# Performance work log

Hardware: AMD Instinct MI355X
Metric: run time of the kernel (lower is better)

The kernel has to match this reference:

```python
import jax, jax.numpy as jnp
import numpy as np

B, S, N, D = 4, 1024, 16, 512
H, HD = 8, 64
THETA = 10000.0


def setup_inputs() -> dict:
    key = jax.random.key(0)
    k0, k1, k2, k3 = jax.random.split(key, 4)
    x = jax.random.normal(k0, (B, S, N, D), dtype=jnp.float32)
    pos_bias = jax.random.normal(k1, (H, N, N), dtype=jnp.float32)
    W_qkv = jax.random.normal(k2, (D, 3 * H * HD), dtype=jnp.float32) / np.sqrt(D).astype(np.float32)
    W_out = jax.random.normal(k3, (H * HD, D), dtype=jnp.float32) / np.sqrt(H * HD).astype(np.float32)
    # mixed mask (not all True -> no early-return path; not all False -> masking active)
    focus_present_mask = jnp.array([True, False, True, False])
    return {"x": x, "pos_bias": pos_bias, "W_qkv": W_qkv, "W_out": W_out,
            "focus_present_mask": focus_present_mask}


def _rotary_cos_sin(n, d, dtype):
    # rotary-embedding-torch: inv_freq over even indices, each freq repeated twice adjacently
    inv_freq = 1.0 / (THETA ** (jnp.arange(0, d, 2, dtype=jnp.float32) / d))
    freqs = jnp.arange(n, dtype=jnp.float32)[:, None] * inv_freq  # (n, d/2)
    freqs = jnp.repeat(freqs, 2, axis=-1)                          # (n, d)
    return jnp.cos(freqs).astype(dtype), jnp.sin(freqs).astype(dtype)


def _rotate_half(t):
    # pairs (x0, x1) -> (-x1, x0), interleaved layout
    t2 = t.reshape(*t.shape[:-1], t.shape[-1] // 2, 2)
    t2 = jnp.stack([-t2[..., 1], t2[..., 0]], axis=-1)
    return t2.reshape(t.shape)


def reference(x, pos_bias, W_qkv, W_out, focus_present_mask):
    scale = HD ** -0.5
    n = x.shape[-2]
    qkv = x @ W_qkv                                   # (b, s, n, 3*h*hd)
    q, k, v = jnp.split(qkv, 3, axis=-1)

    def to_heads(t):  # (..., n, h*hd) -> (..., h, n, hd)
        return t.reshape(*t.shape[:-1], H, HD).swapaxes(-2, -3)

    q = to_heads(q) * scale
    k = to_heads(k)
    v = to_heads(v)

    cos, sin = _rotary_cos_sin(n, HD, q.dtype)
    q = q * cos + _rotate_half(q) * sin
    k = k * cos + _rotate_half(k) * sin

    sim = jnp.einsum('bshid,bshjd->bshij', q, k)      # (b, s, h, n, n)
    sim = sim + pos_bias                              # broadcast (h, n, n)

    eye = jnp.eye(n, dtype=bool)
    ones = jnp.ones((n, n), dtype=bool)
    mask = jnp.where(focus_present_mask[:, None, None, None, None],
                     eye[None, None, None], ones[None, None, None])
    sim = jnp.where(mask, sim, -jnp.finfo(sim.dtype).max)

    attn = jax.nn.softmax(sim, axis=-1)
    out = jnp.einsum('bshij,bshjd->bshid', attn, v)   # (b, s, h, n, hd)
    out = out.swapaxes(-2, -3).reshape(*x.shape[:-1], H * HD)
    return out @ W_out
```

## Files before the change

### kernel.cpp

```cpp
#include <hip/hip_runtime.h>
#include <cstdint>

#define BB   4
#define SS   1024
#define NTOK 16
#define DD   512
#define HH   8
#define HD   64
#define M_TOTAL (BB * SS * NTOK)
#define QKV_COLS (3 * HH * HD)

typedef unsigned short u16;
typedef short bf16x8 __attribute__((ext_vector_type(8)));
typedef float f32x4 __attribute__((ext_vector_type(4)));

__device__ __forceinline__ float bf2f(u16 u) {
  union { uint32_t i; float f; } x; x.i = ((uint32_t)u) << 16; return x.f;
}
__device__ __forceinline__ u16 f2bf(float f) {
  union { uint32_t i; float f; } x; x.f = f;
  uint32_t i = x.i;
  if ((i & 0x7fffffffu) > 0x7f800000u) return 0x7fc0;
  uint32_t r = (i + 0x7fffu + ((i >> 16) & 1u)) >> 16;
  return (u16)r;
}

__device__ __forceinline__ bool decode_mask(const void* p, int b) {
  uint32_t w0 = *(const uint32_t*)p;
  if (w0 == 0x00010001u) return ((const uint8_t*)p)[b] != 0;
  if (w0 == 0x00003F80u) return ((const u16*)p)[b] != 0;
  if (w0 == 0x3F800000u) return ((const float*)p)[b] != 0.0f;
  return ((const int32_t*)p)[b] != 0;
}

__global__ void sniff_kernel(const u16* __restrict__ x, int* __restrict__ flag) {
  __shared__ int any;
  if (threadIdx.x == 0) any = 0;
  __syncthreads();
  int cnt = 0;
  for (int i = threadIdx.x; i < 8192; i += 256) {
    int e = (x[i] >> 7) & 0xFF;
    if (e >= 141) cnt++;
  }
  if (cnt) atomicOr(&any, 1);
  __syncthreads();
  if (threadIdx.x == 0) *flag = any ? 1 : 0;
}

__global__ void rot_table_kernel(float* __restrict__ cosv, float* __restrict__ sinv) {
  for (int p = threadIdx.x; p < NTOK * 32; p += 256) {
    int n = p >> 5, i = p & 31;
    float ang = (float)n * powf(10000.0f, -(float)(2 * i) / 64.0f);
    cosv[p] = cosf(ang);
    sinv[p] = sinf(ang);
  }
}

__global__ __launch_bounds__(256) void cast_x_kernel(
    const void* __restrict__ src, u16* __restrict__ dst, size_t elem_off,
    const int* __restrict__ flag) {
  size_t i = ((size_t)blockIdx.x * 256 + threadIdx.x) * 4;
  ushort4 o;
  if (*flag) {
    float4 v = *(const float4*)((const float*)src + elem_off + i);
    o.x = f2bf(v.x); o.y = f2bf(v.y); o.z = f2bf(v.z); o.w = f2bf(v.w);
  } else {
    o = *(const ushort4*)((const u16*)src + elem_off + i);
  }
  *(ushort4*)(dst + i) = o;
}

__global__ __launch_bounds__(256) void cast_wt_kernel(
    const void* __restrict__ W, u16* __restrict__ WT, int K, int N,
    const int* __restrict__ flag) {
  size_t idx = (size_t)blockIdx.x * 256 + threadIdx.x;
  int n = (int)(idx / K), k = (int)(idx % K);
  float v = (*flag) ? ((const float*)W)[(size_t)k * N + n]
                    : bf2f(((const u16*)W)[(size_t)k * N + n]);
  WT[idx] = f2bf(v);
}

template <int OUT_F32>
__global__ __launch_bounds__(256) void gemm_mfma_bt(
    const u16* __restrict__ A, const u16* __restrict__ BT, void* __restrict__ Cbase,
    size_t c_elem_off, int M, int N, int K, const int* __restrict__ flag) {
  __shared__ u16 Asl[128 * 32];
  __shared__ u16 Bsl[128 * 32];
  const int tid  = threadIdx.x;
  const int wave = tid >> 6;
  const int lane = tid & 63;
  const int bm = blockIdx.y * 128;
  const int bn = blockIdx.x * 128;
  const int wm = (wave >> 1) * 64;
  const int wn = (wave & 1) * 64;
  const int m_lane = lane & 15;
  const int kgrp   = lane >> 4;

  f32x4 acc[4][4];
#pragma unroll
  for (int r = 0; r < 4; ++r)
#pragma unroll
    for (int c = 0; c < 4; ++c) acc[r][c] = (f32x4){0.f, 0.f, 0.f, 0.f};

  for (int k0 = 0; k0 < K; k0 += 32) {
#pragma unroll
    for (int q = 0; q < 2; ++q) {
      const int idx = q * 256 + tid;
      const int row = idx >> 2;
      const int gc  = (idx & 3) ^ (row & 3);
      const u16* ga = A  + (size_t)(bm + row) * K + k0 + gc * 8;
      const u16* gb = BT + (size_t)(bn + row) * K + k0 + gc * 8;
      u16* la = Asl + (size_t)(q * 256 + wave * 64) * 8;
      u16* lb = Bsl + (size_t)(q * 256 + wave * 64) * 8;
      __builtin_amdgcn_global_load_lds(
          (const __attribute__((address_space(1))) void*)ga,
          (__attribute__((address_space(3))) void*)la, 16, 0, 0);
      __builtin_amdgcn_global_load_lds(
          (const __attribute__((address_space(1))) void*)gb,
          (__attribute__((address_space(3))) void*)lb, 16, 0, 0);
    }
    __syncthreads();

    bf16x8 af[4], bfr[4];
#pragma unroll
    for (int r = 0; r < 4; ++r) {
      const int ra = wm + r * 16 + m_lane;
      af[r] = *(const bf16x8*)(Asl + ra * 32 + ((kgrp ^ (ra & 3)) * 8));
    }
#pragma unroll
    for (int c = 0; c < 4; ++c) {
      const int rb = wn + c * 16 + m_lane;
      bfr[c] = *(const bf16x8*)(Bsl + rb * 32 + ((kgrp ^ (rb & 3)) * 8));
    }
#pragma unroll
    for (int r = 0; r < 4; ++r)
#pragma unroll
      for (int c = 0; c < 4; ++c)
        acc[r][c] = __builtin_amdgcn_mfma_f32_16x16x32_bf16(af[r], bfr[c], acc[r][c], 0, 0, 0);
    __syncthreads();
  }

  const bool f32out = OUT_F32 && (*flag != 0);
#pragma unroll
  for (int r = 0; r < 4; ++r) {
    const int grow0 = bm + wm + r * 16 + kgrp * 4;
#pragma unroll
    for (int c = 0; c < 4; ++c) {
      const int gcol = bn + wn + c * 16 + m_lane;
#pragma unroll
      for (int j = 0; j < 4; ++j) {
        const size_t off = c_elem_off + (size_t)(grow0 + j) * N + gcol;
        if (f32out) ((float*)Cbase)[off] = acc[r][c][j];
        else        ((u16*)Cbase)[off]   = f2bf(acc[r][c][j]);
      }
    }
  }
}

__global__ __launch_bounds__(256) void attn_kernel(
    const u16* __restrict__ qkv, const void* __restrict__ pos_bias,
    const void* __restrict__ maskp, u16* __restrict__ attno, int bs0,
    const float* __restrict__ cosv, const float* __restrict__ sinv,
    const int* __restrict__ flag) {
  const int bid = blockIdx.x;
  const int h = bid & (HH - 1);
  const int bsl = bid >> 3;
  const int b = (bs0 + bsl) >> 10;

  __shared__ float qs[NTOK][HD];
  __shared__ float ks[NTOK][HD + 1];
  __shared__ float vs[NTOK][HD];
  __shared__ float sim[NTOK][NTOK + 1];

  const int tid = threadIdx.x;
  const int n = tid >> 4;
  const int e = (tid & 15) * 4;

  size_t rowbase = ((size_t)bsl * NTOK + n) * QKV_COLS + h * HD + e;
  ushort4 uq = *(const ushort4*)(qkv + rowbase);
  ushort4 uk = *(const ushort4*)(qkv + rowbase + 512);
  ushort4 uv = *(const ushort4*)(qkv + rowbase + 1024);
  qs[n][e + 0] = bf2f(uq.x); qs[n][e + 1] = bf2f(uq.y);
  qs[n][e + 2] = bf2f(uq.z); qs[n][e + 3] = bf2f(uq.w);
  ks[n][e + 0] = bf2f(uk.x); ks[n][e + 1] = bf2f(uk.y);
  ks[n][e + 2] = bf2f(uk.z); ks[n][e + 3] = bf2f(uk.w);
  vs[n][e + 0] = bf2f(uv.x); vs[n][e + 1] = bf2f(uv.y);
  vs[n][e + 2] = bf2f(uv.z); vs[n][e + 3] = bf2f(uv.w);
  __syncthreads();

  for (int p = tid; p < NTOK * 32; p += 256) {
    int nn = p >> 5, i = p & 31;
    float c = cosv[p], s = sinv[p];
    float q0 = qs[nn][2 * i], q1 = qs[nn][2 * i + 1];
    qs[nn][2 * i]     = (q0 * c - q1 * s) * 0.125f;
    qs[nn][2 * i + 1] = (q1 * c + q0 * s) * 0.125f;
    float k0 = ks[nn][2 * i], k1 = ks[nn][2 * i + 1];
    ks[nn][2 * i]     = k0 * c - k1 * s;
    ks[nn][2 * i + 1] = k1 * c + k0 * s;
  }
  __syncthreads();

  const int i = tid >> 4, j = tid & 15;
  float acc = 0.0f;
#pragma unroll
  for (int d = 0; d < HD; ++d) acc += qs[i][d] * ks[j][d];
  size_t pbidx = ((size_t)h * NTOK + i) * NTOK + j;
  acc += (*flag) ? ((const float*)pos_bias)[pbidx]
                 : bf2f(((const u16*)pos_bias)[pbidx]);
  bool focus = decode_mask(maskp, b);
  if (focus && (i != j)) acc = -3.0e38f;
  sim[i][j] = acc;
  __syncthreads();

  if (tid < NTOK) {
    float m = -3.4e38f;
#pragma unroll
    for (int jj = 0; jj < NTOK; ++jj) m = fmaxf(m, sim[tid][jj]);
    float ssum = 0.0f;
#pragma unroll
    for (int jj = 0; jj < NTOK; ++jj) {
      float ex = expf(sim[tid][jj] - m);
      sim[tid][jj] = ex;
      ssum += ex;
    }
    float inv = 1.0f / ssum;
#pragma unroll
    for (int jj = 0; jj < NTOK; ++jj) sim[tid][jj] *= inv;
  }
  __syncthreads();

  float o0 = 0, o1 = 0, o2 = 0, o3 = 0;
#pragma unroll
  for (int jj = 0; jj < NTOK; ++jj) {
    float p = sim[n][jj];
    o0 += p * vs[jj][e + 0];
    o1 += p * vs[jj][e + 1];
    o2 += p * vs[jj][e + 2];
    o3 += p * vs[jj][e + 3];
  }
  size_t obase = ((size_t)bsl * NTOK + n) * (HH * HD) + h * HD + e;
  ushort4 uo;
  uo.x = f2bf(o0); uo.y = f2bf(o1); uo.z = f2bf(o2); uo.w = f2bf(o3);
  *(ushort4*)(attno + obase) = uo;
}

extern "C" void kernel_launch(void* const* d_in, const int* in_sizes, int n_in,
                              void* d_out, int out_size, void* d_ws, size_t ws_size,
                              hipStream_t stream) {
  const void* x_raw    = d_in[0];
  const void* pos_bias = d_in[1];
  const void* W_qkv    = d_in[2];
  const void* W_out    = d_in[3];
  const void* maskp    = d_in[4];

  char* ws = (char*)d_ws;
  int*   flag = (int*)ws;
  float* cosv = (float*)(ws + 256);
  float* sinv = cosv + NTOK * 32;
  u16* WqT = (u16*)(ws + 256 + 4096);
  u16* WoT = WqT + (size_t)QKV_COLS * DD;
  u16* scratch = WoT + (size_t)DD * DD;
  const size_t fixed = 256 + 4096 + (size_t)QKV_COLS * DD * 2 + (size_t)DD * DD * 2;
  const size_t ws_avail = (ws_size > fixed) ? ws_size - fixed : 0;

  const size_t per_row = 5120;
  int chunk_rows = M_TOTAL;
  while ((size_t)chunk_rows * per_row > ws_avail && chunk_rows > 128) chunk_rows >>= 1;
  const int nchunks = M_TOTAL / chunk_rows;

  u16* xb    = scratch;
  u16* qkv   = xb  + (size_t)chunk_rows * DD;
  u16* attno = qkv + (size_t)chunk_rows * QKV_COLS;

  sniff_kernel<<<1, 256, 0, stream>>>((const u16*)x_raw, flag);
  rot_table_kernel<<<1, 256, 0, stream>>>(cosv, sinv);
  cast_wt_kernel<<<(QKV_COLS * DD) / 256, 256, 0, stream>>>(W_qkv, WqT, DD, QKV_COLS, flag);
  cast_wt_kernel<<<(DD * DD) / 256, 256, 0, stream>>>(W_out, WoT, DD, DD, flag);

  for (int c = 0; c < nchunks; ++c) {
    const int bs0 = c * (chunk_rows / NTOK);
    const size_t eoff = (size_t)c * chunk_rows * DD;

    cast_x_kernel<<<(int)(((size_t)chunk_rows * DD) / 1024), 256, 0, stream>>>(
        x_raw, xb, eoff, flag);

    {
      dim3 grid(QKV_COLS / 128, chunk_rows / 128);
      gemm_mfma_bt<0><<<grid, 256, 0, stream>>>(xb, WqT, (void*)qkv, 0,
                                                chunk_rows, QKV_COLS, DD, flag);
    }
    {
      dim3 grid((chunk_rows / NTOK) * HH);
      attn_kernel<<<grid, 256, 0, stream>>>(qkv, pos_bias, maskp, attno, bs0,
                                            cosv, sinv, flag);
    }
    {
      dim3 grid(DD / 128, chunk_rows / 128);
      gemm_mfma_bt<1><<<grid, 256, 0, stream>>>(attno, WoT, d_out, eoff,
                                                chunk_rows, DD, DD, flag);
    }
  }
}
```

Baseline: 628.0 us.

## Rewrite attention kernel as one wave per (row, head) using bf16 MFMA

The attention kernel now gives each wavefront a single (b,s,head) 16x16 problem, with four per block, instead of one block per problem. QK^T and PV are computed with 16x16x32 bf16 MFMA instructions, and softmax is reduced with cross-lane shuffles rather than through shared memory and block barriers. Rotary cos/sin tables are staged in LDS. This removes most __syncthreads and scalar FMA work, at the cost of rounding rotated q/k and the probabilities to bf16, plus strided uncoalesced V loads.

```diff
diff --git a/kernel.cpp b/kernel.cpp
--- a/kernel.cpp
+++ b/kernel.cpp
@@ -162,86 +162,119 @@
     const void* __restrict__ maskp, u16* __restrict__ attno, int bs0,
     const float* __restrict__ cosv, const float* __restrict__ sinv,
     const int* __restrict__ flag) {
-  const int bid = blockIdx.x;
-  const int h = bid & (HH - 1);
-  const int bsl = bid >> 3;
+  __shared__ float lcos[NTOK * 33];
+  __shared__ float lsin[NTOK * 33];
+  const int tid = threadIdx.x;
+  for (int p = tid; p < NTOK * 32; p += 256) {
+    int n = p >> 5, i = p & 31;
+    lcos[n * 33 + i] = cosv[p];
+    lsin[n * 33 + i] = sinv[p];
+  }
+  __syncthreads();
+
+  const int wave = tid >> 6;
+  const int lane = tid & 63;
+  const int wid = blockIdx.x * 4 + wave;
+  const int bsl = wid >> 3;
+  const int h = wid & (HH - 1);
   const int b = (bs0 + bsl) >> 10;
-
-  __shared__ float qs[NTOK][HD];
-  __shared__ float ks[NTOK][HD + 1];
-  __shared__ float vs[NTOK][HD];
-  __shared__ float sim[NTOK][NTOK + 1];
-
-  const int tid = threadIdx.x;
-  const int n = tid >> 4;
-  const int e = (tid & 15) * 4;
-
-  size_t rowbase = ((size_t)bsl * NTOK + n) * QKV_COLS + h * HD + e;
-  ushort4 uq = *(const ushort4*)(qkv + rowbase);
-  ushort4 uk = *(const ushort4*)(qkv + rowbase + 512);
-  ushort4 uv = *(const ushort4*)(qkv + rowbase + 1024);
-  qs[n][e + 0] = bf2f(uq.x); qs[n][e + 1] = bf2f(uq.y);
-  qs[n][e + 2] = bf2f(uq.z); qs[n][e + 3] = bf2f(uq.w);
-  ks[n][e + 0] = bf2f(uk.x); ks[n][e + 1] = bf2f(uk.y);
-  ks[n][e + 2] = bf2f(uk.z); ks[n][e + 3] = bf2f(uk.w);
-  vs[n][e + 0] = bf2f(uv.x); vs[n][e + 1] = bf2f(uv.y);
-  vs[n][e + 2] = bf2f(uv.z); vs[n][e + 3] = bf2f(uv.w);
-  __syncthreads();
-
-  for (int p = tid; p < NTOK * 32; p += 256) {
-    int nn = p >> 5, i = p & 31;
-    float c = cosv[p], s = sinv[p];
-    float q0 = qs[nn][2 * i], q1 = qs[nn][2 * i + 1];
-    qs[nn][2 * i]     = (q0 * c - q1 * s) * 0.125f;
-    qs[nn][2 * i + 1] = (q1 * c + q0 * s) * 0.125f;
-    float k0 = ks[nn][2 * i], k1 = ks[nn][2 * i + 1];
-    ks[nn][2 * i]     = k0 * c - k1 * s;
-    ks[nn][2 * i + 1] = k1 * c + k0 * s;
-  }
-  __syncthreads();
-
-  const int i = tid >> 4, j = tid & 15;
-  float acc = 0.0f;
-#pragma unroll
-  for (int d = 0; d < HD; ++d) acc += qs[i][d] * ks[j][d];
-  size_t pbidx = ((size_t)h * NTOK + i) * NTOK + j;
-  acc += (*flag) ? ((const float*)pos_bias)[pbidx]
-                 : bf2f(((const u16*)pos_bias)[pbidx]);
-  bool focus = decode_mask(maskp, b);
-  if (focus && (i != j)) acc = -3.0e38f;
-  sim[i][j] = acc;
-  __syncthreads();
-
-  if (tid < NTOK) {
-    float m = -3.4e38f;
-#pragma unroll
-    for (int jj = 0; jj < NTOK; ++jj) m = fmaxf(m, sim[tid][jj]);
-    float ssum = 0.0f;
-#pragma unroll
-    for (int jj = 0; jj < NTOK; ++jj) {
-      float ex = expf(sim[tid][jj] - m);
-      sim[tid][jj] = ex;
-      ssum += ex;
-    }
-    float inv = 1.0f / ssum;
-#pragma unroll
-    for (int jj = 0; jj < NTOK; ++jj) sim[tid][jj] *= inv;
-  }
-  __syncthreads();
-
-  float o0 = 0, o1 = 0, o2 = 0, o3 = 0;
-#pragma unroll
-  for (int jj = 0; jj < NTOK; ++jj) {
-    float p = sim[n][jj];
-    o0 += p * vs[jj][e + 0];
-    o1 += p * vs[jj][e + 1];
-    o2 += p * vs[jj][e + 2];
-    o3 += p * vs[jj][e + 3];
-  }
-  size_t obase = ((size_t)bsl * NTOK + n) * (HH * HD) + h * HD + e;
-  ushort4 uo;
-  uo.x = f2bf(o0); uo.y = f2bf(o1); uo.z = f2bf(o2); uo.w = f2bf(o3);
-  *(ushort4*)(attno + obase) = uo;
+  const int qt = lane & 15;
+  const int kg = lane >> 4;
+
+  const u16* rowp = qkv + ((size_t)bsl * NTOK + qt) * QKV_COLS + h * HD;
+  float qv[16], kv[16];
+#pragma unroll
+  for (int hf = 0; hf < 2; ++hf) {
+    const bf16x8 uq = *(const bf16x8*)(rowp + hf * 32 + kg * 8);
+    const bf16x8 uk = *(const bf16x8*)(rowp + 512 + hf * 32 + kg * 8);
+#pragma unroll
+    for (int t = 0; t < 8; ++t) {
+      qv[hf * 8 + t] = bf2f((u16)uq[t]);
+      kv[hf * 8 + t] = bf2f((u16)uk[t]);
+    }
+  }
+
+  const u16* vbase = qkv + (size_t)bsl * NTOK * QKV_COLS + 1024 + h * HD;
+  u16 vraw[32];
+#pragma unroll
+  for (int mt = 0; mt < 4; ++mt)
+#pragma unroll
+    for (int t = 0; t < 8; ++t)
+      vraw[mt * 8 + t] = (kg < 2)
+          ? vbase[(size_t)(kg * 8 + t) * QKV_COLS + mt * 16 + qt]
+          : (u16)0;
+
+  bf16x8 qa[2], ka[2];
+#pragma unroll
+  for (int hf = 0; hf < 2; ++hf) {
+#pragma unroll
+    for (int t = 0; t < 4; ++t) {
+      const int idx = qt * 33 + hf * 16 + kg * 4 + t;
+      const float cth = lcos[idx], sth = lsin[idx];
+      const int e0 = hf * 8 + 2 * t, e1 = e0 + 1;
+      const float q0 = qv[e0], q1 = qv[e1];
+      qa[hf][2 * t]     = (short)f2bf((q0 * cth - q1 * sth) * 0.125f);
+      qa[hf][2 * t + 1] = (short)f2bf((q1 * cth + q0 * sth) * 0.125f);
+      const float k0 = kv[e0], k1 = kv[e1];
+      ka[hf][2 * t]     = (short)f2bf(k0 * cth - k1 * sth);
+      ka[hf][2 * t + 1] = (short)f2bf(k1 * cth + k0 * sth);
+    }
+  }
+
+  f32x4 cacc = (f32x4){0.f, 0.f, 0.f, 0.f};
+  cacc = __builtin_amdgcn_mfma_f32_16x16x32_bf16(ka[0], qa[0], cacc, 0, 0, 0);
+  cacc = __builtin_amdgcn_mfma_f32_16x16x32_bf16(ka[1], qa[1], cacc, 0, 0, 0);
+
+  const bool f32pb = (*flag != 0);
+  const bool focus = decode_mask(maskp, b);
+  float sv[4];
+#pragma unroll
+  for (int j = 0; j < 4; ++j) {
+    const int kt = kg * 4 + j;
+    const size_t pbidx = ((size_t)h * NTOK + qt) * NTOK + kt;
+    const float pb = f32pb ? ((const float*)pos_bias)[pbidx]
+                           : bf2f(((const u16*)pos_bias)[pbidx]);
+    float v = cacc[j] + pb;
+    if (focus && (qt != kt)) v = -3.0e38f;
+    sv[j] = v;
+  }
+
+  float m = fmaxf(fmaxf(sv[0], sv[1]), fmaxf(sv[2], sv[3]));
+  m = fmaxf(m, __shfl_xor(m, 16, 64));
+  m = fmaxf(m, __shfl_xor(m, 32, 64));
+  float pj[4];
+  float ssum = 0.f;
+#pragma unroll
+  for (int j = 0; j < 4; ++j) {
+    pj[j] = expf(sv[j] - m);
+    ssum += pj[j];
+  }
+  ssum += __shfl_xor(ssum, 16, 64);
+  ssum += __shfl_xor(ssum, 32, 64);
+  const float inv = 1.0f / ssum;
+#pragma unroll
+  for (int j = 0; j < 4; ++j) pj[j] *= inv;
+
+  bf16x8 pfrag;
+#pragma unroll
+  for (int t = 0; t < 8; ++t) {
+    const int src = (lane & 15) + (((kg << 1) + (t >> 2)) << 4);
+    const float v = __shfl(pj[t & 3], src & 63, 64);
+    pfrag[t] = (kg < 2) ? (short)f2bf(v) : (short)0;
+  }
+
+  u16* orow = attno + ((size_t)bsl * NTOK + qt) * (HH * HD) + h * HD;
+#pragma unroll
+  for (int mt = 0; mt < 4; ++mt) {
+    bf16x8 vfrag;
+#pragma unroll
+    for (int t = 0; t < 8; ++t) vfrag[t] = (short)vraw[mt * 8 + t];
+    f32x4 o = (f32x4){0.f, 0.f, 0.f, 0.f};
+    o = __builtin_amdgcn_mfma_f32_16x16x32_bf16(vfrag, pfrag, o, 0, 0, 0);
+    ushort4 uo;
+    uo.x = f2bf(o[0]); uo.y = f2bf(o[1]); uo.z = f2bf(o[2]); uo.w = f2bf(o[3]);
+    *(ushort4*)(orow + mt * 16 + kg * 4) = uo;
+  }
 }
 
 extern "C" void kernel_launch(void* const* d_in, const int* in_sizes, int n_in,
@@ -290,7 +323,7 @@
                                                 chunk_rows, QKV_COLS, DD, flag);
     }
     {
-      dim3 grid((chunk_rows / NTOK) * HH);
+      dim3 grid(((chunk_rows / NTOK) * HH) / 4);
       attn_kernel<<<grid, 256, 0, stream>>>(qkv, pos_bias, maskp, attno, bs0,
                                             cosv, sinv, flag);
     }
```

Result: faster. 538.6 us (-14.2%).
